# Kernel optimization log

Hardware: AMD Instinct MI355X
Metric: run time of the kernel (lower is better)

Reference implementation:

```python
import jax, jax.numpy as jnp
import numpy as np

N_LIG, M_POC = 16384, 32768
E_LIG, E_POC, K_CROSS = 163840, 327680, 8
H = 64
L = 4

silu = jax.nn.silu


def _lin(k, fan_in, fan_out):
    k1, k2 = jax.random.split(k)
    s = 1.0 / np.sqrt(fan_in)
    W = jax.random.uniform(k1, (fan_in, fan_out), jnp.float32, -s, s)
    b = jax.random.uniform(k2, (fan_out,), jnp.float32, -s, s)
    return W, b


def setup_inputs() -> dict:
    key = jax.random.key(0)
    ks = jax.random.split(key, 32)
    inp = {
        'lig_x': jax.random.normal(ks[0], (N_LIG, 3), jnp.float32),
        'lig_h': jax.random.normal(ks[1], (N_LIG, 17), jnp.float32),
        'poc_x': jax.random.normal(ks[2], (M_POC, 3), jnp.float32),
        'poc_h': jax.random.normal(ks[3], (M_POC, 29), jnp.float32),
        'lig_edge_index': jax.random.randint(ks[4], (2, E_LIG), 0, N_LIG, jnp.int32),
        'lig_edge_attr': jax.random.normal(ks[5], (E_LIG, 6), jnp.float32),
        'poc_edge_index': jax.random.randint(ks[6], (2, E_POC), 0, M_POC, jnp.int32),
        'poc_edge_attr': jax.random.normal(ks[7], (E_POC, 16), jnp.float32),
        'cross_edge_index': jnp.stack([
            jax.random.randint(ks[8], (N_LIG * K_CROSS,), 0, M_POC, jnp.int32),
            jax.random.randint(ks[9], (N_LIG * K_CROSS,), 0, N_LIG, jnp.int32)]),
        'cross_edge_attr': jax.random.normal(ks[10], (N_LIG * K_CROSS, 16), jnp.float32),
        't': jax.random.uniform(ks[11], (1,), jnp.float32),
    }
    # embeddings
    inp['lig_emb_W'], inp['lig_emb_b'] = _lin(ks[12], 18, H)
    inp['poc_emb_W'], inp['poc_emb_b'] = _lin(ks[13], 29, H)
    inp['lig_ee_W'], inp['lig_ee_b'] = _lin(ks[14], 6, H)
    inp['poc_ee_W'], inp['poc_ee_b'] = _lin(ks[15], 16, H)
    inp['cross_ee_W'], inp['cross_ee_b'] = _lin(ks[16], 16, H)
    # per-layer params stacked along leading L axis
    def stack(kk, fan_in, fan_out):
        Ws, bs = zip(*[_lin(k, fan_in, fan_out) for k in jax.random.split(kk, L)])
        return jnp.stack(Ws), jnp.stack(bs)
    inp['phi_e_W1'], inp['phi_e_b1'] = stack(ks[17], 2 * H + 1 + H, H)
    inp['phi_e_W2'], inp['phi_e_b2'] = stack(ks[18], H, H)
    inp['phi_x_W1'], inp['phi_x_b1'] = stack(ks[19], H, H)
    inp['phi_x_W2'], inp['phi_x_b2'] = stack(ks[20], H, 1)
    inp['phi_h_W1'], inp['phi_h_b1'] = stack(ks[21], 2 * H, H)
    inp['phi_h_W2'], inp['phi_h_b2'] = stack(ks[22], H, H)
    inp['out_W1'], inp['out_b1'] = _lin(ks[23], H, H)
    inp['out_W2'], inp['out_b2'] = _lin(ks[24], H, 1)
    return inp


def _forward(lig_x, lig_h, poc_x, poc_h, lig_edge_attr, poc_edge_attr,
             cross_edge_attr, t,
             lig_emb_W, lig_emb_b, poc_emb_W, poc_emb_b,
             lig_ee_W, lig_ee_b, poc_ee_W, poc_ee_b, cross_ee_W, cross_ee_b,
             phi_e_W1, phi_e_b1, phi_e_W2, phi_e_b2,
             phi_x_W1, phi_x_b1, phi_x_W2, phi_x_b2,
             phi_h_W1, phi_h_b1, phi_h_W2, phi_h_b2,
             out_W1, out_b1, out_W2, out_b2,
             lig_edge_index, poc_edge_index, cross_edge_index):
    n_lig = lig_h.shape[0]
    n_tot = n_lig + poc_h.shape[0]
    t_feat = jnp.broadcast_to(t.reshape(1, 1), (n_lig, 1))
    h_lig = jnp.concatenate([lig_h, t_feat], -1) @ lig_emb_W + lig_emb_b
    h_poc = poc_h @ poc_emb_W + poc_emb_b
    h = jnp.concatenate([h_lig, h_poc], 0)          # [N, H]
    x = jnp.concatenate([lig_x, poc_x], 0)          # [N, 3]
    src = jnp.concatenate([lig_edge_index[0], poc_edge_index[0] + n_lig,
                           cross_edge_index[0] + n_lig])
    dst = jnp.concatenate([lig_edge_index[1], poc_edge_index[1] + n_lig,
                           cross_edge_index[1]])
    eattr = jnp.concatenate([
        lig_edge_attr @ lig_ee_W + lig_ee_b,
        poc_edge_attr @ poc_ee_W + poc_ee_b,
        cross_edge_attr @ cross_ee_W + cross_ee_b], 0)  # [E, H]
    # True = pocket => coords not updated
    update_mask = jnp.concatenate([
        jnp.ones((n_lig, 1), h.dtype), jnp.zeros((n_tot - n_lig, 1), h.dtype)], 0)
    for i in range(phi_e_W1.shape[0]):
        diff = x[src] - x[dst]                                    # [E, 3]
        dist = jnp.sum(diff * diff, -1, keepdims=True) / 100.0    # [E, 1]
        e_in = jnp.concatenate([h[src], h[dst], dist, eattr], -1) # [E, 2H+1+H]
        m = silu(silu(e_in @ phi_e_W1[i] + phi_e_b1[i]) @ phi_e_W2[i] + phi_e_b2[i])
        cw = jnp.tanh(silu(m @ phi_x_W1[i] + phi_x_b1[i]) @ phi_x_W2[i] + phi_x_b2[i])
        coord_agg = jax.ops.segment_sum(diff * cw, dst, num_segments=n_tot) * update_mask
        msg_agg = jax.ops.segment_sum(m, dst, num_segments=n_tot)
        h = h + silu(jnp.concatenate([h, msg_agg], -1) @ phi_h_W1[i] + phi_h_b1[i]) @ phi_h_W2[i] + phi_h_b2[i]
        x = x + coord_agg
    disp = x[:n_lig] - lig_x
    scale = silu(h[:n_lig] @ out_W1 + out_b1) @ out_W2 + out_b2
    return scale * disp


def reference(lig_x, lig_h, poc_x, poc_h, lig_edge_attr, poc_edge_attr,
              cross_edge_attr, t,
              lig_emb_W, lig_emb_b, poc_emb_W, poc_emb_b,
              lig_ee_W, lig_ee_b, poc_ee_W, poc_ee_b, cross_ee_W, cross_ee_b,
              phi_e_W1, phi_e_b1, phi_e_W2, phi_e_b2,
              phi_x_W1, phi_x_b1, phi_x_W2, phi_x_b2,
              phi_h_W1, phi_h_b1, phi_h_W2, phi_h_b2,
              out_W1, out_b1, out_W2, out_b2,
              lig_edge_index, poc_edge_index, cross_edge_index):
    return _forward(lig_x, lig_h, poc_x, poc_h, lig_edge_attr, poc_edge_attr,
                    cross_edge_attr, t,
                    lig_emb_W, lig_emb_b, poc_emb_W, poc_emb_b,
                    lig_ee_W, lig_ee_b, poc_ee_W, poc_ee_b, cross_ee_W, cross_ee_b,
                    phi_e_W1, phi_e_b1, phi_e_W2, phi_e_b2,
                    phi_x_W1, phi_x_b1, phi_x_W2, phi_x_b2,
                    phi_h_W1, phi_h_b1, phi_h_W2, phi_h_b2,
                    out_W1, out_b1, out_W2, out_b2,
                    lig_edge_index, poc_edge_index, cross_edge_index)
```

## Files before the change

kernel.cpp:

```cpp
#include <hip/hip_runtime.h>

#define N_LIG 16384
#define M_POC 32768
#define N_TOT (N_LIG + M_POC)
#define E_LIG 163840
#define E_POC 327680
#define E_CROSS (N_LIG * 8)
#define E_TOT (E_LIG + E_POC + E_CROSS)
#define TE 16

typedef __bf16 bf16_t;
typedef bf16_t bf16x8 __attribute__((ext_vector_type(8)));
typedef bf16_t bf16x4 __attribute__((ext_vector_type(4)));
typedef bf16_t bf16x2 __attribute__((ext_vector_type(2)));
typedef float f32x4 __attribute__((ext_vector_type(4)));

#define SM 72
#define WAVE_BYTES (1792 + 2304 + 2304 + 256)

__device__ __forceinline__ float fast_rcp(float x) { return __builtin_amdgcn_rcpf(x); }
__device__ __forceinline__ float silu_f(float v) {
    return v * fast_rcp(1.0f + __expf(-v));
}
__device__ __forceinline__ float tanh_f(float v) {
    float a = fabsf(v);
    float t = __expf(-2.0f * a);
    float r = (1.0f - t) * fast_rcp(1.0f + t);
    return copysignf(r, v);
}

__device__ __forceinline__ void atomic_add_f32(float* p, float v) {
    __hip_atomic_fetch_add(p, v, __ATOMIC_RELAXED, __HIP_MEMORY_SCOPE_AGENT);
}

__device__ __forceinline__ void lds_fence() {
    asm volatile("s_waitcnt lgkmcnt(0)" ::: "memory");
}


__global__ void k_build_edges(const int* __restrict__ lig_ei, const int* __restrict__ poc_ei,
                              const int* __restrict__ cross_ei,
                              int* __restrict__ srcA, int* __restrict__ dstA,
                              int* __restrict__ cnt) {
    int e = blockIdx.x * blockDim.x + threadIdx.x;
    if (e >= E_TOT) return;
    int s, d;
    if (e < E_LIG) {
        s = lig_ei[e];
        d = lig_ei[E_LIG + e];
    } else if (e < E_LIG + E_POC) {
        int i = e - E_LIG;
        s = poc_ei[i] + N_LIG;
        d = poc_ei[E_POC + i] + N_LIG;
    } else {
        int i = e - E_LIG - E_POC;
        s = cross_ei[i] + N_LIG;
        d = cross_ei[E_CROSS + i];
    }
    srcA[e] = s;
    dstA[e] = d;
    atomicAdd(&cnt[d], 1);
}

__global__ __launch_bounds__(1024) void k_scan(const int* __restrict__ cnt,
                                               int* __restrict__ rowptr,
                                               int* __restrict__ cursor) {
    __shared__ int sums[1024];
    int tid = threadIdx.x;
    int local[48];
    int s = 0;
    for (int i = 0; i < 48; ++i) { local[i] = s; s += cnt[tid * 48 + i]; }
    sums[tid] = s;
    __syncthreads();
    for (int off = 1; off < 1024; off <<= 1) {
        int v = (tid >= off) ? sums[tid - off] : 0;
        __syncthreads();
        sums[tid] += v;
        __syncthreads();
    }
    int base = (tid == 0) ? 0 : sums[tid - 1];
    for (int i = 0; i < 48; ++i) {
        int v = base + local[i];
        int idx = tid * 48 + i;
        rowptr[idx] = v;
        cursor[idx] = v;
    }
    if (tid == 1023) rowptr[N_TOT] = sums[1023];
}

__global__ void k_scatter(const int* __restrict__ dstA, int* __restrict__ cursor,
                          int* __restrict__ sortedPos) {
    int e = blockIdx.x * blockDim.x + threadIdx.x;
    if (e < E_TOT) sortedPos[e] = atomicAdd(&cursor[dstA[e]], 1);
}

#define PK_G1   (12 * 5 * 4 * 64)
#define PK_G23  (4 * 4 * 4 * 64)
#define PK_WH   (4 * 24 * 64)
#define PK_BEFF (12 * 64)
#define PK_TOT  (PK_G1 + PK_G23 + PK_WH + PK_BEFF)

__global__ void k_pack_all(const float* __restrict__ phi_e_W1, const float* __restrict__ phi_e_b1,
                           const float* __restrict__ lig_ee_W, const float* __restrict__ lig_ee_b,
                           const float* __restrict__ poc_ee_W, const float* __restrict__ poc_ee_b,
                           const float* __restrict__ cross_ee_W, const float* __restrict__ cross_ee_b,
                           const float* __restrict__ phi_e_W2, const float* __restrict__ phi_x_W1,
                           const float* __restrict__ phi_h_W1, const float* __restrict__ phi_h_W2,
                           bf16_t* __restrict__ Bg1, bf16_t* __restrict__ Bg23,
                           bf16_t* __restrict__ WhP, float* __restrict__ beff) {
    int tid = blockIdx.x * blockDim.x + threadIdx.x;
    if (tid < PK_G1) {
        int lt = tid / 1280;
        int rem = tid - lt * 1280;
        int c = rem >> 8;
        int ft = (rem >> 6) & 3;
        int lane = rem & 63;
        int l = lt / 3, t = lt % 3;
        const float* W1l = phi_e_W1 + l * 193 * 64;
        const float* We; int K;
        if (t == 0) { We = lig_ee_W; K = 6; }
        else if (t == 1) { We = poc_ee_W; K = 16; }
        else { We = cross_ee_W; K = 16; }
        int col = ft * 16 + (lane & 15);
        int k0 = c * 32 + (lane >> 4) * 8;
        #pragma unroll
        for (int j = 0; j < 8; ++j) {
            int row = k0 + j;
            float v = 0.0f;
            if (row < 128) v = W1l[row * 64 + col];
            else if (row < 144) {
                int kk = row - 128;
                if (kk < K) {
                    float a = 0.0f;
                    for (int q = 0; q < 64; ++q) a = fmaf(We[kk * 64 + q], W1l[(129 + q) * 64 + col], a);
                    v = a;
                }
            } else if (row == 144) {
                v = W1l[128 * 64 + col];
            }
            Bg1[(size_t)tid * 8 + j] = (bf16_t)v;
        }
    } else if (tid < PK_G1 + PK_G23) {
        int u = tid - PK_G1;
        int lane = u & 63;
        int ft = (u >> 6) & 3;
        int c = (u >> 8) & 3;
        int l = u >> 10;
        const float* W = (c < 2) ? (phi_e_W2 + l * 4096) : (phi_x_W1 + l * 4096);
        int kb = (c & 1) * 32;
        int col = ft * 16 + (lane & 15);
        int k0 = kb + (lane >> 4) * 8;
        #pragma unroll
        for (int j = 0; j < 8; ++j)
            Bg23[(size_t)u * 8 + j] = (bf16_t)W[(k0 + j) * 64 + col];
    } else if (tid < PK_G1 + PK_G23 + PK_WH) {
        int u = tid - PK_G1 - PK_G23;
        int lane = u & 63;
        int frag = (u >> 6) % 24;
        int l = (u >> 6) / 24;
        const float* W; int kc, ft;
        if (frag < 16) { W = phi_h_W1 + l * 128 * 64; kc = frag >> 2; ft = frag & 3; }
        else           { W = phi_h_W2 + l * 64 * 64;  kc = (frag - 16) >> 2; ft = (frag - 16) & 3; }
        int col = ft * 16 + (lane & 15);
        int k0 = kc * 32 + (lane >> 4) * 8;
        #pragma unroll
        for (int j = 0; j < 8; ++j)
            WhP[(size_t)u * 8 + j] = (bf16_t)W[(k0 + j) * 64 + col];
    } else if (tid < PK_TOT) {
        int u = tid - PK_G1 - PK_G23 - PK_WH;
        int j = u & 63;
        int lt = u >> 6;
        int l = lt / 3, t = lt % 3;
        const float* W1l = phi_e_W1 + l * 193 * 64;
        const float* Be = (t == 0) ? lig_ee_b : ((t == 1) ? poc_ee_b : cross_ee_b);
        float v = phi_e_b1[l * 64 + j];
        for (int q = 0; q < 64; ++q) v = fmaf(Be[q], W1l[(129 + q) * 64 + j], v);
        beff[u] = v;
    }
}

__global__ void k_embed(const float* __restrict__ lig_x, const float* __restrict__ lig_h,
                        const float* __restrict__ poc_x, const float* __restrict__ poc_h,
                        const float* __restrict__ t,
                        const float* __restrict__ ligW, const float* __restrict__ ligB,
                        const float* __restrict__ pocW, const float* __restrict__ pocB,
                        float* __restrict__ h, bf16_t* __restrict__ hB, float* __restrict__ x4) {
    int gid = blockIdx.x * blockDim.x + threadIdx.x;
    int n = gid >> 6;
    int lane = gid & 63;
    if (n >= N_TOT) return;
    float a;
    if (n < N_LIG) {
        a = ligB[lane];
        #pragma unroll
        for (int k = 0; k < 17; ++k) a = fmaf(lig_h[n * 17 + k], ligW[k * 64 + lane], a);
        a = fmaf(t[0], ligW[17 * 64 + lane], a);
        if (lane < 4) x4[n * 4 + lane] = (lane < 3) ? lig_x[n * 3 + lane] : 0.0f;
    } else {
        int p = n - N_LIG;
        a = pocB[lane];
        #pragma unroll
        for (int k = 0; k < 29; ++k) a = fmaf(poc_h[p * 29 + k], pocW[k * 64 + lane], a);
        if (lane < 4) x4[n * 4 + lane] = (lane < 3) ? poc_x[p * 3 + lane] : 0.0f;
    }
    h[n * 64 + lane] = a;
    hB[n * 64 + lane] = (bf16_t)a;
}

__global__ __launch_bounds__(256, 6) void k_edge_mfma(
    const bf16_t* __restrict__ hB, const float* __restrict__ x4,
    const int* __restrict__ srcA, const int* __restrict__ dstA,
    const int* __restrict__ sortedPos,
    const float* __restrict__ lig_attr, const float* __restrict__ poc_attr,
    const float* __restrict__ cross_attr,
    const bf16_t* __restrict__ Bg1L,
    const float* __restrict__ beffL,
    const bf16_t* __restrict__ Bg23L,
    const float* __restrict__ b2, const float* __restrict__ bx1,
    const float* __restrict__ Wx2, const float* __restrict__ bx2,
    bf16_t* __restrict__ mBuf, float* __restrict__ coord_agg) {
    __shared__ __align__(16) char lds[4 * WAVE_BYTES];
    const int lane = threadIdx.x & 63;
    const int wave = threadIdx.x >> 6;
    bf16_t* exL = (bf16_t*)(lds + wave * WAVE_BYTES);
    bf16_t* mT1 = (bf16_t*)(lds + wave * WAVE_BYTES + 1792);
    bf16_t* mT2 = (bf16_t*)(lds + wave * WAVE_BYTES + 1792 + 2304);
    float*  dfL = (float*)(lds + wave * WAVE_BYTES + 1792 + 2304 + 2304);
    const int base = (blockIdx.x * 4 + wave) * TE;

    int tt; const float* attrBase; int astride;
    if (base < E_LIG) { tt = 0; attrBase = lig_attr + (size_t)base * 6; astride = 6; }
    else if (base < E_LIG + E_POC) { tt = 1; attrBase = poc_attr + (size_t)(base - E_LIG) * 16; astride = 16; }
    else { tt = 2; attrBase = cross_attr + (size_t)(base - E_LIG - E_POC) * 16; astride = 16; }

    const int edge = lane & 15;
    const int kgrp = lane >> 4;
    const int mrow0 = kgrp * 4;
    const int e16 = base + edge;
    const int sv = srcA[e16];
    const int dv = dstA[e16];
    const int sp = sortedPos[e16];

    bf16x8 bf0 = *(const bf16x8*)(hB + (size_t)sv * 64 + kgrp * 8);
    bf16x8 bf1 = *(const bf16x8*)(hB + (size_t)sv * 64 + 32 + kgrp * 8);
    bf16x8 bf2 = *(const bf16x8*)(hB + (size_t)dv * 64 + kgrp * 8);
    bf16x8 bf3 = *(const bf16x8*)(hB + (size_t)dv * 64 + 32 + kgrp * 8);

    {
        bf16x8 z = {(bf16_t)0.f, (bf16_t)0.f, (bf16_t)0.f, (bf16_t)0.f,
                    (bf16_t)0.f, (bf16_t)0.f, (bf16_t)0.f, (bf16_t)0.f};
        *(bf16x8*)(exL + (lane >> 2) * 56 + (lane & 3) * 8) = z;
    }
    lds_fence();
    if (lane < 16) {
        float4 xs = *(const float4*)(x4 + (size_t)sv * 4);
        float4 xd = *(const float4*)(x4 + (size_t)dv * 4);
        float d0 = xs.x - xd.x;
        float d1 = xs.y - xd.y;
        float d2 = xs.z - xd.z;
        float dist = (d0 * d0 + d1 * d1 + d2 * d2) * 0.01f;
        exL[lane * 56 + 16] = (bf16_t)dist;
        *(float4*)(dfL + lane * 4) = (float4){d0, d1, d2, dist};
        const float* attr = attrBase + lane * astride;
        if (tt == 0) {
            float2 a0 = *(const float2*)(attr);
            float2 a1 = *(const float2*)(attr + 2);
            float2 a2 = *(const float2*)(attr + 4);
            bf16x8 w0 = {(bf16_t)a0.x, (bf16_t)a0.y, (bf16_t)a1.x, (bf16_t)a1.y,
                         (bf16_t)a2.x, (bf16_t)a2.y, (bf16_t)0.f, (bf16_t)0.f};
            *(bf16x8*)(exL + lane * 56) = w0;
        } else {
            float4 a0 = *(const float4*)(attr);
            float4 a1 = *(const float4*)(attr + 4);
            float4 a2 = *(const float4*)(attr + 8);
            float4 a3 = *(const float4*)(attr + 12);
            bf16x8 w0 = {(bf16_t)a0.x, (bf16_t)a0.y, (bf16_t)a0.z, (bf16_t)a0.w,
                         (bf16_t)a1.x, (bf16_t)a1.y, (bf16_t)a1.z, (bf16_t)a1.w};
            bf16x8 w1 = {(bf16_t)a2.x, (bf16_t)a2.y, (bf16_t)a2.z, (bf16_t)a2.w,
                         (bf16_t)a3.x, (bf16_t)a3.y, (bf16_t)a3.z, (bf16_t)a3.w};
            *(bf16x8*)(exL + lane * 56) = w0;
            *(bf16x8*)(exL + lane * 56 + 8) = w1;
        }
    }
    lds_fence();

    const bf16_t* Bg1 = Bg1L + (size_t)tt * 5 * 4 * 512;
    const float* beff = beffL + tt * 64;
    f32x4 acc1[4];
    #pragma unroll
    for (int ft = 0; ft < 4; ++ft) {
        float4 bv = *(const float4*)(beff + ft * 16 + mrow0);
        acc1[ft] = (f32x4){bv.x, bv.y, bv.z, bv.w};
    }
    bf16x8 bf4 = *(const bf16x8*)(exL + edge * 56 + kgrp * 8);
    bf16x8 bdat[5] = {bf0, bf1, bf2, bf3, bf4};
    #pragma unroll
    for (int c = 0; c < 5; ++c) {
        #pragma unroll
        for (int ft = 0; ft < 4; ++ft) {
            bf16x8 wfr = *(const bf16x8*)(Bg1 + ((size_t)(c * 4 + ft) * 64 + lane) * 8);
            acc1[ft] = __builtin_amdgcn_mfma_f32_16x16x32_bf16(wfr, bdat[c], acc1[ft], 0, 0, 0);
        }
    }
    #pragma unroll
    for (int ft = 0; ft < 4; ++ft) {
        bf16x4 v = {(bf16_t)silu_f(acc1[ft][0]), (bf16_t)silu_f(acc1[ft][1]),
                    (bf16_t)silu_f(acc1[ft][2]), (bf16_t)silu_f(acc1[ft][3])};
        *(bf16x4*)(mT1 + edge * SM + ft * 16 + mrow0) = v;
    }
    lds_fence();

    f32x4 acc2[4];
    #pragma unroll
    for (int ft = 0; ft < 4; ++ft) {
        float4 bv = *(const float4*)(b2 + ft * 16 + mrow0);
        acc2[ft] = (f32x4){bv.x, bv.y, bv.z, bv.w};
    }
    bf16x8 m1f0 = *(const bf16x8*)(mT1 + edge * SM + kgrp * 8);
    bf16x8 m1f1 = *(const bf16x8*)(mT1 + edge * SM + 32 + kgrp * 8);
    #pragma unroll
    for (int c = 0; c < 2; ++c) {
        bf16x8 df = (c == 0) ? m1f0 : m1f1;
        #pragma unroll
        for (int ft = 0; ft < 4; ++ft) {
            bf16x8 wfr = *(const bf16x8*)(Bg23L + ((size_t)(c * 4 + ft) * 64 + lane) * 8);
            acc2[ft] = __builtin_amdgcn_mfma_f32_16x16x32_bf16(wfr, df, acc2[ft], 0, 0, 0);
        }
    }
    #pragma unroll
    for (int ft = 0; ft < 4; ++ft) {
        bf16x4 v = {(bf16_t)silu_f(acc2[ft][0]), (bf16_t)silu_f(acc2[ft][1]),
                    (bf16_t)silu_f(acc2[ft][2]), (bf16_t)silu_f(acc2[ft][3])};
        *(bf16x4*)(mT2 + edge * SM + ft * 16 + mrow0) = v;
        *(bf16x4*)(mBuf + (size_t)sp * 64 + ft * 16 + mrow0) = v;
    }
    lds_fence();

    f32x4 acc3[4];
    #pragma unroll
    for (int ft = 0; ft < 4; ++ft) {
        float4 bv = *(const float4*)(bx1 + ft * 16 + mrow0);
        acc3[ft] = (f32x4){bv.x, bv.y, bv.z, bv.w};
    }
    bf16x8 mf0 = *(const bf16x8*)(mT2 + edge * SM + kgrp * 8);
    bf16x8 mf1 = *(const bf16x8*)(mT2 + edge * SM + 32 + kgrp * 8);
    const bf16_t* Bg3 = Bg23L + (size_t)2 * 4 * 512;
    #pragma unroll
    for (int c = 0; c < 2; ++c) {
        bf16x8 df = (c == 0) ? mf0 : mf1;
        #pragma unroll
        for (int ft = 0; ft < 4; ++ft) {
            bf16x8 wfr = *(const bf16x8*)(Bg3 + ((size_t)(c * 4 + ft) * 64 + lane) * 8);
            acc3[ft] = __builtin_amdgcn_mfma_f32_16x16x32_bf16(wfr, df, acc3[ft], 0, 0, 0);
        }
    }

    float s = 0.0f;
    #pragma unroll
    for (int ft = 0; ft < 4; ++ft) {
        float4 wv = *(const float4*)(Wx2 + ft * 16 + mrow0);
        s = fmaf(silu_f(acc3[ft][0]), wv.x, s);
        s = fmaf(silu_f(acc3[ft][1]), wv.y, s);
        s = fmaf(silu_f(acc3[ft][2]), wv.z, s);
        s = fmaf(silu_f(acc3[ft][3]), wv.w, s);
    }
    s += __shfl_xor(s, 16, 64);
    s += __shfl_xor(s, 32, 64);
    const float cw = tanh_f(s + bx2[0]);
    if (dv < N_LIG && kgrp < 3)
        atomic_add_f32(&coord_agg[dv * 3 + kgrp], dfL[edge * 4 + kgrp] * cw);
}

#define NODE_WAVE_BYTES (2304 + 2304)
__global__ __launch_bounds__(256) void k_node(
    float* __restrict__ h, bf16_t* __restrict__ hB, float* __restrict__ x4,
    const bf16_t* __restrict__ mBuf, const int* __restrict__ rowptr,
    float* __restrict__ coord,
    const bf16_t* __restrict__ WhL,
    const float* __restrict__ bh1, const float* __restrict__ bh2) {
    __shared__ __align__(16) char lds[4 * NODE_WAVE_BYTES];
    const int lane = threadIdx.x & 63;
    const int wave = threadIdx.x >> 6;
    bf16_t* msgT = (bf16_t*)(lds + wave * NODE_WAVE_BYTES);
    bf16_t* mid  = (bf16_t*)(lds + wave * NODE_WAVE_BYTES + 2304);
    const int base = (blockIdx.x * 4 + wave) * TE;

    const int node = lane & 15;
    const int kgrp = lane >> 4;
    const int mrow0 = kgrp * 4;
    const int n16 = base + node;

    const int rp0 = rowptr[n16];
    const int rp1 = rowptr[n16 + 1];
    const int f4 = node * 4;
    for (int r = 0; r < TE; ++r) {
        const int s0 = __shfl(rp0, r, 64);
        const int s1 = __shfl(rp1, r, 64);
        float a0 = 0.f, a1 = 0.f, a2 = 0.f, a3 = 0.f;
        for (int i = s0 + kgrp; i < s1; i += 4) {
            bf16x4 v = *(const bf16x4*)(mBuf + (size_t)i * 64 + f4);
            a0 += (float)v[0]; a1 += (float)v[1]; a2 += (float)v[2]; a3 += (float)v[3];
        }
        a0 += __shfl_xor(a0, 16, 64); a1 += __shfl_xor(a1, 16, 64);
        a2 += __shfl_xor(a2, 16, 64); a3 += __shfl_xor(a3, 16, 64);
        a0 += __shfl_xor(a0, 32, 64); a1 += __shfl_xor(a1, 32, 64);
        a2 += __shfl_xor(a2, 32, 64); a3 += __shfl_xor(a3, 32, 64);
        if (lane < 16) {
            bf16x4 v = {(bf16_t)a0, (bf16_t)a1, (bf16_t)a2, (bf16_t)a3};
            *(bf16x4*)(msgT + r * SM + f4) = v;
        }
    }
    lds_fence();

    f32x4 acc[4];
    #pragma unroll
    for (int ft = 0; ft < 4; ++ft) {
        float4 bv = *(const float4*)(bh1 + ft * 16 + mrow0);
        acc[ft] = (f32x4){bv.x, bv.y, bv.z, bv.w};
    }
    bf16x8 d0 = *(const bf16x8*)(hB + (size_t)n16 * 64 + kgrp * 8);
    bf16x8 d1 = *(const bf16x8*)(hB + (size_t)n16 * 64 + 32 + kgrp * 8);
    bf16x8 d2 = *(const bf16x8*)(msgT + node * SM + kgrp * 8);
    bf16x8 d3 = *(const bf16x8*)(msgT + node * SM + 32 + kgrp * 8);
    bf16x8 bdat[4] = {d0, d1, d2, d3};
    #pragma unroll
    for (int c = 0; c < 4; ++c) {
        #pragma unroll
        for (int ft = 0; ft < 4; ++ft) {
            bf16x8 wfr = *(const bf16x8*)(WhL + ((size_t)(c * 4 + ft) * 64 + lane) * 8);
            acc[ft] = __builtin_amdgcn_mfma_f32_16x16x32_bf16(wfr, bdat[c], acc[ft], 0, 0, 0);
        }
    }
    #pragma unroll
    for (int ft = 0; ft < 4; ++ft) {
        bf16x4 v = {(bf16_t)silu_f(acc[ft][0]), (bf16_t)silu_f(acc[ft][1]),
                    (bf16_t)silu_f(acc[ft][2]), (bf16_t)silu_f(acc[ft][3])};
        *(bf16x4*)(mid + node * SM + ft * 16 + mrow0) = v;
    }
    lds_fence();

    f32x4 acc2[4];
    #pragma unroll
    for (int ft = 0; ft < 4; ++ft) {
        float4 bv = *(const float4*)(bh2 + ft * 16 + mrow0);
        acc2[ft] = (f32x4){bv.x, bv.y, bv.z, bv.w};
    }
    bf16x8 g0 = *(const bf16x8*)(mid + node * SM + kgrp * 8);
    bf16x8 g1 = *(const bf16x8*)(mid + node * SM + 32 + kgrp * 8);
    #pragma unroll
    for (int c = 0; c < 2; ++c) {
        bf16x8 df = (c == 0) ? g0 : g1;
        #pragma unroll
        for (int ft = 0; ft < 4; ++ft) {
            bf16x8 wfr = *(const bf16x8*)(WhL + ((size_t)(16 + c * 4 + ft) * 64 + lane) * 8);
            acc2[ft] = __builtin_amdgcn_mfma_f32_16x16x32_bf16(wfr, df, acc2[ft], 0, 0, 0);
        }
    }

    #pragma unroll
    for (int ft = 0; ft < 4; ++ft) {
        float* hp = h + (size_t)n16 * 64 + ft * 16 + mrow0;
        float4 hv = *(const float4*)hp;
        hv.x += acc2[ft][0]; hv.y += acc2[ft][1]; hv.z += acc2[ft][2]; hv.w += acc2[ft][3];
        *(float4*)hp = hv;
        bf16x4 hb = {(bf16_t)hv.x, (bf16_t)hv.y, (bf16_t)hv.z, (bf16_t)hv.w};
        *(bf16x4*)(hB + (size_t)n16 * 64 + ft * 16 + mrow0) = hb;
    }
    if (kgrp < 3) {
        if (n16 < N_LIG) x4[n16 * 4 + kgrp] += coord[n16 * 3 + kgrp];
        coord[n16 * 3 + kgrp] = 0.0f;
    }
}

__global__ void k_out(const float* __restrict__ h, const float* __restrict__ x4,
                      const float* __restrict__ lig_x,
                      const float* __restrict__ oW1, const float* __restrict__ ob1,
                      const float* __restrict__ oW2, const float* __restrict__ ob2,
                      float* __restrict__ out) {
    int gid = blockIdx.x * blockDim.x + threadIdx.x;
    int n = gid >> 6;
    int lane = gid & 63;
    if (n >= N_LIG) return;
    float hv = h[n * 64 + lane];
    float a = ob1[lane];
    #pragma unroll
    for (int k = 0; k < 64; ++k) a = fmaf(__shfl(hv, k, 64), oW1[k * 64 + lane], a);
    float p = silu_f(a) * oW2[lane];
    #pragma unroll
    for (int off = 32; off > 0; off >>= 1) p += __shfl_xor(p, off, 64);
    float scale = p + ob2[0];
    if (lane < 3) out[n * 3 + lane] = scale * (x4[n * 4 + lane] - lig_x[n * 3 + lane]);
}

extern "C" void kernel_launch(void* const* d_in, const int* in_sizes, int n_in,
                              void* d_out, int out_size, void* d_ws, size_t ws_size,
                              hipStream_t stream) {
    const float* lig_x      = (const float*)d_in[0];
    const float* lig_h      = (const float*)d_in[1];
    const float* poc_x      = (const float*)d_in[2];
    const float* poc_h      = (const float*)d_in[3];
    const int*   lig_ei     = (const int*)d_in[4];
    const float* lig_attr   = (const float*)d_in[5];
    const int*   poc_ei     = (const int*)d_in[6];
    const float* poc_attr   = (const float*)d_in[7];
    const int*   cross_ei   = (const int*)d_in[8];
    const float* cross_attr = (const float*)d_in[9];
    const float* t          = (const float*)d_in[10];
    const float* lig_emb_W  = (const float*)d_in[11];
    const float* lig_emb_b  = (const float*)d_in[12];
    const float* poc_emb_W  = (const float*)d_in[13];
    const float* poc_emb_b  = (const float*)d_in[14];
    const float* lig_ee_W   = (const float*)d_in[15];
    const float* lig_ee_b   = (const float*)d_in[16];
    const float* poc_ee_W   = (const float*)d_in[17];
    const float* poc_ee_b   = (const float*)d_in[18];
    const float* cross_ee_W = (const float*)d_in[19];
    const float* cross_ee_b = (const float*)d_in[20];
    const float* phi_e_W1   = (const float*)d_in[21];
    const float* phi_e_b1   = (const float*)d_in[22];
    const float* phi_e_W2   = (const float*)d_in[23];
    const float* phi_e_b2   = (const float*)d_in[24];
    const float* phi_x_W1   = (const float*)d_in[25];
    const float* phi_x_b1   = (const float*)d_in[26];
    const float* phi_x_W2   = (const float*)d_in[27];
    const float* phi_x_b2   = (const float*)d_in[28];
    const float* phi_h_W1   = (const float*)d_in[29];
    const float* phi_h_b1   = (const float*)d_in[30];
    const float* phi_h_W2   = (const float*)d_in[31];
    const float* phi_h_b2   = (const float*)d_in[32];
    const float* out_W1     = (const float*)d_in[33];
    const float* out_b1     = (const float*)d_in[34];
    const float* out_W2     = (const float*)d_in[35];
    const float* out_b2     = (const float*)d_in[36];

    char* p = (char*)d_ws;
    auto carve = [&](size_t bytes) { char* r = p; p += (bytes + 255) & ~(size_t)255; return r; };
    float*  h      = (float*)carve((size_t)N_TOT * 64 * 4);
    bf16_t* hB     = (bf16_t*)carve((size_t)N_TOT * 64 * 2);
    float*  x4     = (float*)carve((size_t)N_TOT * 4 * 4);
    float*  coord  = (float*)carve((size_t)N_TOT * 3 * 4);
    bf16_t* WhP    = (bf16_t*)carve((size_t)4 * 24 * 512 * 2);
    float*  beff   = (float*)carve((size_t)12 * 64 * 4);
    bf16_t* Bg1    = (bf16_t*)carve((size_t)12 * 5 * 4 * 512 * 2);
    bf16_t* Bg23   = (bf16_t*)carve((size_t)4 * 16 * 512 * 2);
    int*    srcA   = (int*)carve((size_t)E_TOT * 4);
    int*    dstA   = (int*)carve((size_t)E_TOT * 4);
    int*    sortedPos = (int*)carve((size_t)E_TOT * 4);
    int*    cnt    = (int*)carve((size_t)N_TOT * 4);
    int*    cursor = (int*)carve((size_t)N_TOT * 4);
    int*    rowptr = (int*)carve((size_t)(N_TOT + 1) * 4);
    bf16_t* mBuf   = (bf16_t*)carve((size_t)E_TOT * 64 * 2);

    hipMemsetAsync(cnt, 0, (size_t)N_TOT * 4, stream);
    hipMemsetAsync(coord, 0, (size_t)N_TOT * 3 * 4, stream);
    k_build_edges<<<E_TOT / 256, 256, 0, stream>>>(lig_ei, poc_ei, cross_ei, srcA, dstA, cnt);
    k_scan<<<1, 1024, 0, stream>>>(cnt, rowptr, cursor);
    k_scatter<<<E_TOT / 256, 256, 0, stream>>>(dstA, cursor, sortedPos);
    k_pack_all<<<(PK_TOT + 255) / 256, 256, 0, stream>>>(
        phi_e_W1, phi_e_b1, lig_ee_W, lig_ee_b, poc_ee_W, poc_ee_b, cross_ee_W, cross_ee_b,
        phi_e_W2, phi_x_W1, phi_h_W1, phi_h_W2, Bg1, Bg23, WhP, beff);
    k_embed<<<(N_TOT * 64) / 256, 256, 0, stream>>>(
        lig_x, lig_h, poc_x, poc_h, t, lig_emb_W, lig_emb_b, poc_emb_W, poc_emb_b, h, hB, x4);

    for (int l = 0; l < 4; ++l) {
        k_edge_mfma<<<E_TOT / 64, 256, 0, stream>>>(
            hB, x4, srcA, dstA, sortedPos, lig_attr, poc_attr, cross_attr,
            Bg1 + (size_t)l * 3 * 5 * 4 * 512, beff + (size_t)l * 3 * 64,
            Bg23 + (size_t)l * 16 * 512,
            phi_e_b2 + l * 64, phi_x_b1 + l * 64,
            phi_x_W2 + l * 64, phi_x_b2 + l,
            mBuf, coord);
        k_node<<<N_TOT / 64, 256, 0, stream>>>(
            h, hB, x4, mBuf, rowptr, coord,
            WhP + (size_t)l * 24 * 512,
            phi_h_b1 + l * 64, phi_h_b2 + l * 64);
    }

    k_out<<<(N_LIG * 64) / 256, 256, 0, stream>>>(
        h, x4, lig_x, out_W1, out_b1, out_W2, out_b2, (float*)d_out);
}
```

Baseline: 858.4 us.

## Process two 16-edge tiles per wave and keep edge features in registers

Each wave in the edge kernel now handles 32 edges as two interleaved MFMA tiles, so every weight fragment load feeds two MFMAs. Edge attributes and distances are built directly in registers and exchanged by shuffle instead of being staged in LDS, and message stores to the sorted buffer become wider. The grid is halved and the occupancy hint is lowered to 4 to allow for the extra registers, which may reduce latency hiding.

```diff
diff --git a/kernel.cpp b/kernel.cpp
--- a/kernel.cpp
+++ b/kernel.cpp
@@ -12,11 +12,10 @@
 typedef __bf16 bf16_t;
 typedef bf16_t bf16x8 __attribute__((ext_vector_type(8)));
 typedef bf16_t bf16x4 __attribute__((ext_vector_type(4)));
-typedef bf16_t bf16x2 __attribute__((ext_vector_type(2)));
 typedef float f32x4 __attribute__((ext_vector_type(4)));
 
 #define SM 72
-#define WAVE_BYTES (1792 + 2304 + 2304 + 256)
+#define EDGE_WAVE_BYTES (32 * SM * 2)
 
 __device__ __forceinline__ float fast_rcp(float x) { return __builtin_amdgcn_rcpf(x); }
 __device__ __forceinline__ float silu_f(float v) {
@@ -207,7 +206,7 @@
     hB[n * 64 + lane] = (bf16_t)a;
 }
 
-__global__ __launch_bounds__(256, 6) void k_edge_mfma(
+__global__ __launch_bounds__(256, 4) void k_edge_mfma(
     const bf16_t* __restrict__ hB, const float* __restrict__ x4,
     const int* __restrict__ srcA, const int* __restrict__ dstA,
     const int* __restrict__ sortedPos,
@@ -219,14 +218,11 @@
     const float* __restrict__ b2, const float* __restrict__ bx1,
     const float* __restrict__ Wx2, const float* __restrict__ bx2,
     bf16_t* __restrict__ mBuf, float* __restrict__ coord_agg) {
-    __shared__ __align__(16) char lds[4 * WAVE_BYTES];
+    __shared__ __align__(16) char lds[4 * EDGE_WAVE_BYTES];
     const int lane = threadIdx.x & 63;
     const int wave = threadIdx.x >> 6;
-    bf16_t* exL = (bf16_t*)(lds + wave * WAVE_BYTES);
-    bf16_t* mT1 = (bf16_t*)(lds + wave * WAVE_BYTES + 1792);
-    bf16_t* mT2 = (bf16_t*)(lds + wave * WAVE_BYTES + 1792 + 2304);
-    float*  dfL = (float*)(lds + wave * WAVE_BYTES + 1792 + 2304 + 2304);
-    const int base = (blockIdx.x * 4 + wave) * TE;
+    bf16_t* mT = (bf16_t*)(lds + wave * EDGE_WAVE_BYTES);
+    const int base = (blockIdx.x * 4 + wave) * 32;
 
     int tt; const float* attrBase; int astride;
     if (base < E_LIG) { tt = 0; attrBase = lig_attr + (size_t)base * 6; astride = 6; }
@@ -236,139 +232,197 @@
     const int edge = lane & 15;
     const int kgrp = lane >> 4;
     const int mrow0 = kgrp * 4;
-    const int e16 = base + edge;
-    const int sv = srcA[e16];
-    const int dv = dstA[e16];
-    const int sp = sortedPos[e16];
-
-    bf16x8 bf0 = *(const bf16x8*)(hB + (size_t)sv * 64 + kgrp * 8);
-    bf16x8 bf1 = *(const bf16x8*)(hB + (size_t)sv * 64 + 32 + kgrp * 8);
-    bf16x8 bf2 = *(const bf16x8*)(hB + (size_t)dv * 64 + kgrp * 8);
-    bf16x8 bf3 = *(const bf16x8*)(hB + (size_t)dv * 64 + 32 + kgrp * 8);
-
-    {
-        bf16x8 z = {(bf16_t)0.f, (bf16_t)0.f, (bf16_t)0.f, (bf16_t)0.f,
-                    (bf16_t)0.f, (bf16_t)0.f, (bf16_t)0.f, (bf16_t)0.f};
-        *(bf16x8*)(exL + (lane >> 2) * 56 + (lane & 3) * 8) = z;
-    }
-    lds_fence();
-    if (lane < 16) {
-        float4 xs = *(const float4*)(x4 + (size_t)sv * 4);
-        float4 xd = *(const float4*)(x4 + (size_t)dv * 4);
-        float d0 = xs.x - xd.x;
-        float d1 = xs.y - xd.y;
-        float d2 = xs.z - xd.z;
-        float dist = (d0 * d0 + d1 * d1 + d2 * d2) * 0.01f;
-        exL[lane * 56 + 16] = (bf16_t)dist;
-        *(float4*)(dfL + lane * 4) = (float4){d0, d1, d2, dist};
-        const float* attr = attrBase + lane * astride;
+    const int e0 = base + edge;
+    const int e1 = base + 16 + edge;
+    const int sv0 = srcA[e0], sv1 = srcA[e1];
+    const int dv0 = dstA[e0], dv1 = dstA[e1];
+    const int sp0 = sortedPos[e0], sp1 = sortedPos[e1];
+
+    bf16x8 hs0a = *(const bf16x8*)(hB + (size_t)sv0 * 64 + kgrp * 8);
+    bf16x8 hs0b = *(const bf16x8*)(hB + (size_t)sv0 * 64 + 32 + kgrp * 8);
+    bf16x8 hd0a = *(const bf16x8*)(hB + (size_t)dv0 * 64 + kgrp * 8);
+    bf16x8 hd0b = *(const bf16x8*)(hB + (size_t)dv0 * 64 + 32 + kgrp * 8);
+    bf16x8 hs1a = *(const bf16x8*)(hB + (size_t)sv1 * 64 + kgrp * 8);
+    bf16x8 hs1b = *(const bf16x8*)(hB + (size_t)sv1 * 64 + 32 + kgrp * 8);
+    bf16x8 hd1a = *(const bf16x8*)(hB + (size_t)dv1 * 64 + kgrp * 8);
+    bf16x8 hd1b = *(const bf16x8*)(hB + (size_t)dv1 * 64 + 32 + kgrp * 8);
+
+    const bf16_t Z = (bf16_t)0.0f;
+    bf16x8 ex0 = {Z, Z, Z, Z, Z, Z, Z, Z};
+    bf16x8 ex1 = {Z, Z, Z, Z, Z, Z, Z, Z};
+    float d0s0 = 0.f, d1s0 = 0.f, d2s0 = 0.f;
+    float d0s1 = 0.f, d1s1 = 0.f, d2s1 = 0.f;
+    if (kgrp == 0) {
+        const float* a0p = attrBase + (size_t)edge * astride;
+        const float* a1p = attrBase + (size_t)(16 + edge) * astride;
         if (tt == 0) {
-            float2 a0 = *(const float2*)(attr);
-            float2 a1 = *(const float2*)(attr + 2);
-            float2 a2 = *(const float2*)(attr + 4);
-            bf16x8 w0 = {(bf16_t)a0.x, (bf16_t)a0.y, (bf16_t)a1.x, (bf16_t)a1.y,
-                         (bf16_t)a2.x, (bf16_t)a2.y, (bf16_t)0.f, (bf16_t)0.f};
-            *(bf16x8*)(exL + lane * 56) = w0;
+            float4 q0 = *(const float4*)a0p;
+            float2 q1 = *(const float2*)(a0p + 4);
+            ex0 = (bf16x8){(bf16_t)q0.x, (bf16_t)q0.y, (bf16_t)q0.z, (bf16_t)q0.w,
+                           (bf16_t)q1.x, (bf16_t)q1.y, Z, Z};
+            float4 r0 = *(const float4*)a1p;
+            float2 r1 = *(const float2*)(a1p + 4);
+            ex1 = (bf16x8){(bf16_t)r0.x, (bf16_t)r0.y, (bf16_t)r0.z, (bf16_t)r0.w,
+                           (bf16_t)r1.x, (bf16_t)r1.y, Z, Z};
         } else {
-            float4 a0 = *(const float4*)(attr);
-            float4 a1 = *(const float4*)(attr + 4);
-            float4 a2 = *(const float4*)(attr + 8);
-            float4 a3 = *(const float4*)(attr + 12);
-            bf16x8 w0 = {(bf16_t)a0.x, (bf16_t)a0.y, (bf16_t)a0.z, (bf16_t)a0.w,
-                         (bf16_t)a1.x, (bf16_t)a1.y, (bf16_t)a1.z, (bf16_t)a1.w};
-            bf16x8 w1 = {(bf16_t)a2.x, (bf16_t)a2.y, (bf16_t)a2.z, (bf16_t)a2.w,
-                         (bf16_t)a3.x, (bf16_t)a3.y, (bf16_t)a3.z, (bf16_t)a3.w};
-            *(bf16x8*)(exL + lane * 56) = w0;
-            *(bf16x8*)(exL + lane * 56 + 8) = w1;
-        }
-    }
-    lds_fence();
+            float4 q0 = *(const float4*)a0p;
+            float4 q1 = *(const float4*)(a0p + 4);
+            ex0 = (bf16x8){(bf16_t)q0.x, (bf16_t)q0.y, (bf16_t)q0.z, (bf16_t)q0.w,
+                           (bf16_t)q1.x, (bf16_t)q1.y, (bf16_t)q1.z, (bf16_t)q1.w};
+            float4 r0 = *(const float4*)a1p;
+            float4 r1 = *(const float4*)(a1p + 4);
+            ex1 = (bf16x8){(bf16_t)r0.x, (bf16_t)r0.y, (bf16_t)r0.z, (bf16_t)r0.w,
+                           (bf16_t)r1.x, (bf16_t)r1.y, (bf16_t)r1.z, (bf16_t)r1.w};
+        }
+    } else if (kgrp == 1) {
+        if (tt != 0) {
+            const float* a0p = attrBase + (size_t)edge * astride + 8;
+            const float* a1p = attrBase + (size_t)(16 + edge) * astride + 8;
+            float4 q0 = *(const float4*)a0p;
+            float4 q1 = *(const float4*)(a0p + 4);
+            ex0 = (bf16x8){(bf16_t)q0.x, (bf16_t)q0.y, (bf16_t)q0.z, (bf16_t)q0.w,
+                           (bf16_t)q1.x, (bf16_t)q1.y, (bf16_t)q1.z, (bf16_t)q1.w};
+            float4 r0 = *(const float4*)a1p;
+            float4 r1 = *(const float4*)(a1p + 4);
+            ex1 = (bf16x8){(bf16_t)r0.x, (bf16_t)r0.y, (bf16_t)r0.z, (bf16_t)r0.w,
+                           (bf16_t)r1.x, (bf16_t)r1.y, (bf16_t)r1.z, (bf16_t)r1.w};
+        }
+    } else if (kgrp == 2) {
+        float4 xs0 = *(const float4*)(x4 + (size_t)sv0 * 4);
+        float4 xd0 = *(const float4*)(x4 + (size_t)dv0 * 4);
+        float4 xs1 = *(const float4*)(x4 + (size_t)sv1 * 4);
+        float4 xd1 = *(const float4*)(x4 + (size_t)dv1 * 4);
+        d0s0 = xs0.x - xd0.x; d1s0 = xs0.y - xd0.y; d2s0 = xs0.z - xd0.z;
+        d0s1 = xs1.x - xd1.x; d1s1 = xs1.y - xd1.y; d2s1 = xs1.z - xd1.z;
+        float dist0 = (d0s0 * d0s0 + d1s0 * d1s0 + d2s0 * d2s0) * 0.01f;
+        float dist1 = (d0s1 * d0s1 + d1s1 * d1s1 + d2s1 * d2s1) * 0.01f;
+        ex0[0] = (bf16_t)dist0;
+        ex1[0] = (bf16_t)dist1;
+    }
 
     const bf16_t* Bg1 = Bg1L + (size_t)tt * 5 * 4 * 512;
     const float* beff = beffL + tt * 64;
-    f32x4 acc1[4];
+    f32x4 acc0[4], acc1[4];
     #pragma unroll
     for (int ft = 0; ft < 4; ++ft) {
         float4 bv = *(const float4*)(beff + ft * 16 + mrow0);
-        acc1[ft] = (f32x4){bv.x, bv.y, bv.z, bv.w};
-    }
-    bf16x8 bf4 = *(const bf16x8*)(exL + edge * 56 + kgrp * 8);
-    bf16x8 bdat[5] = {bf0, bf1, bf2, bf3, bf4};
+        acc0[ft] = (f32x4){bv.x, bv.y, bv.z, bv.w};
+        acc1[ft] = acc0[ft];
+    }
+    bf16x8 bdat0[5] = {hs0a, hs0b, hd0a, hd0b, ex0};
+    bf16x8 bdat1[5] = {hs1a, hs1b, hd1a, hd1b, ex1};
     #pragma unroll
     for (int c = 0; c < 5; ++c) {
         #pragma unroll
         for (int ft = 0; ft < 4; ++ft) {
             bf16x8 wfr = *(const bf16x8*)(Bg1 + ((size_t)(c * 4 + ft) * 64 + lane) * 8);
-            acc1[ft] = __builtin_amdgcn_mfma_f32_16x16x32_bf16(wfr, bdat[c], acc1[ft], 0, 0, 0);
-        }
-    }
-    #pragma unroll
-    for (int ft = 0; ft < 4; ++ft) {
-        bf16x4 v = {(bf16_t)silu_f(acc1[ft][0]), (bf16_t)silu_f(acc1[ft][1]),
-                    (bf16_t)silu_f(acc1[ft][2]), (bf16_t)silu_f(acc1[ft][3])};
-        *(bf16x4*)(mT1 + edge * SM + ft * 16 + mrow0) = v;
+            acc0[ft] = __builtin_amdgcn_mfma_f32_16x16x32_bf16(wfr, bdat0[c], acc0[ft], 0, 0, 0);
+            acc1[ft] = __builtin_amdgcn_mfma_f32_16x16x32_bf16(wfr, bdat1[c], acc1[ft], 0, 0, 0);
+        }
+    }
+    #pragma unroll
+    for (int ft = 0; ft < 4; ++ft) {
+        bf16x4 v0 = {(bf16_t)silu_f(acc0[ft][0]), (bf16_t)silu_f(acc0[ft][1]),
+                     (bf16_t)silu_f(acc0[ft][2]), (bf16_t)silu_f(acc0[ft][3])};
+        bf16x4 v1 = {(bf16_t)silu_f(acc1[ft][0]), (bf16_t)silu_f(acc1[ft][1]),
+                     (bf16_t)silu_f(acc1[ft][2]), (bf16_t)silu_f(acc1[ft][3])};
+        *(bf16x4*)(mT + edge * SM + ft * 16 + mrow0) = v0;
+        *(bf16x4*)(mT + (16 + edge) * SM + ft * 16 + mrow0) = v1;
     }
     lds_fence();
 
-    f32x4 acc2[4];
+    f32x4 acc20[4], acc21[4];
     #pragma unroll
     for (int ft = 0; ft < 4; ++ft) {
         float4 bv = *(const float4*)(b2 + ft * 16 + mrow0);
-        acc2[ft] = (f32x4){bv.x, bv.y, bv.z, bv.w};
-    }
-    bf16x8 m1f0 = *(const bf16x8*)(mT1 + edge * SM + kgrp * 8);
-    bf16x8 m1f1 = *(const bf16x8*)(mT1 + edge * SM + 32 + kgrp * 8);
+        acc20[ft] = (f32x4){bv.x, bv.y, bv.z, bv.w};
+        acc21[ft] = acc20[ft];
+    }
+    bf16x8 m10[2], m11[2];
     #pragma unroll
     for (int c = 0; c < 2; ++c) {
-        bf16x8 df = (c == 0) ? m1f0 : m1f1;
+        m10[c] = *(const bf16x8*)(mT + edge * SM + c * 32 + kgrp * 8);
+        m11[c] = *(const bf16x8*)(mT + (16 + edge) * SM + c * 32 + kgrp * 8);
+    }
+    #pragma unroll
+    for (int c = 0; c < 2; ++c) {
         #pragma unroll
         for (int ft = 0; ft < 4; ++ft) {
             bf16x8 wfr = *(const bf16x8*)(Bg23L + ((size_t)(c * 4 + ft) * 64 + lane) * 8);
-            acc2[ft] = __builtin_amdgcn_mfma_f32_16x16x32_bf16(wfr, df, acc2[ft], 0, 0, 0);
-        }
-    }
-    #pragma unroll
-    for (int ft = 0; ft < 4; ++ft) {
-        bf16x4 v = {(bf16_t)silu_f(acc2[ft][0]), (bf16_t)silu_f(acc2[ft][1]),
-                    (bf16_t)silu_f(acc2[ft][2]), (bf16_t)silu_f(acc2[ft][3])};
-        *(bf16x4*)(mT2 + edge * SM + ft * 16 + mrow0) = v;
-        *(bf16x4*)(mBuf + (size_t)sp * 64 + ft * 16 + mrow0) = v;
+            acc20[ft] = __builtin_amdgcn_mfma_f32_16x16x32_bf16(wfr, m10[c], acc20[ft], 0, 0, 0);
+            acc21[ft] = __builtin_amdgcn_mfma_f32_16x16x32_bf16(wfr, m11[c], acc21[ft], 0, 0, 0);
+        }
     }
     lds_fence();
-
-    f32x4 acc3[4];
+    #pragma unroll
+    for (int ft = 0; ft < 4; ++ft) {
+        bf16x4 v0 = {(bf16_t)silu_f(acc20[ft][0]), (bf16_t)silu_f(acc20[ft][1]),
+                     (bf16_t)silu_f(acc20[ft][2]), (bf16_t)silu_f(acc20[ft][3])};
+        bf16x4 v1 = {(bf16_t)silu_f(acc21[ft][0]), (bf16_t)silu_f(acc21[ft][1]),
+                     (bf16_t)silu_f(acc21[ft][2]), (bf16_t)silu_f(acc21[ft][3])};
+        *(bf16x4*)(mT + edge * SM + ft * 16 + mrow0) = v0;
+        *(bf16x4*)(mT + (16 + edge) * SM + ft * 16 + mrow0) = v1;
+    }
+    lds_fence();
+
+    bf16x8 g0[2], g1[2];
+    #pragma unroll
+    for (int c = 0; c < 2; ++c) {
+        g0[c] = *(const bf16x8*)(mT + edge * SM + c * 32 + kgrp * 8);
+        g1[c] = *(const bf16x8*)(mT + (16 + edge) * SM + c * 32 + kgrp * 8);
+        *(bf16x8*)(mBuf + (size_t)sp0 * 64 + c * 32 + kgrp * 8) = g0[c];
+        *(bf16x8*)(mBuf + (size_t)sp1 * 64 + c * 32 + kgrp * 8) = g1[c];
+    }
+
+    f32x4 acc30[4], acc31[4];
     #pragma unroll
     for (int ft = 0; ft < 4; ++ft) {
         float4 bv = *(const float4*)(bx1 + ft * 16 + mrow0);
-        acc3[ft] = (f32x4){bv.x, bv.y, bv.z, bv.w};
-    }
-    bf16x8 mf0 = *(const bf16x8*)(mT2 + edge * SM + kgrp * 8);
-    bf16x8 mf1 = *(const bf16x8*)(mT2 + edge * SM + 32 + kgrp * 8);
+        acc30[ft] = (f32x4){bv.x, bv.y, bv.z, bv.w};
+        acc31[ft] = acc30[ft];
+    }
     const bf16_t* Bg3 = Bg23L + (size_t)2 * 4 * 512;
     #pragma unroll
     for (int c = 0; c < 2; ++c) {
-        bf16x8 df = (c == 0) ? mf0 : mf1;
         #pragma unroll
         for (int ft = 0; ft < 4; ++ft) {
             bf16x8 wfr = *(const bf16x8*)(Bg3 + ((size_t)(c * 4 + ft) * 64 + lane) * 8);
-            acc3[ft] = __builtin_amdgcn_mfma_f32_16x16x32_bf16(wfr, df, acc3[ft], 0, 0, 0);
-        }
-    }
-
-    float s = 0.0f;
+            acc30[ft] = __builtin_amdgcn_mfma_f32_16x16x32_bf16(wfr, g0[c], acc30[ft], 0, 0, 0);
+            acc31[ft] = __builtin_amdgcn_mfma_f32_16x16x32_bf16(wfr, g1[c], acc31[ft], 0, 0, 0);
+        }
+    }
+
+    float s0 = 0.0f, s1 = 0.0f;
     #pragma unroll
     for (int ft = 0; ft < 4; ++ft) {
         float4 wv = *(const float4*)(Wx2 + ft * 16 + mrow0);
-        s = fmaf(silu_f(acc3[ft][0]), wv.x, s);
-        s = fmaf(silu_f(acc3[ft][1]), wv.y, s);
-        s = fmaf(silu_f(acc3[ft][2]), wv.z, s);
-        s = fmaf(silu_f(acc3[ft][3]), wv.w, s);
-    }
-    s += __shfl_xor(s, 16, 64);
-    s += __shfl_xor(s, 32, 64);
-    const float cw = tanh_f(s + bx2[0]);
-    if (dv < N_LIG && kgrp < 3)
-        atomic_add_f32(&coord_agg[dv * 3 + kgrp], dfL[edge * 4 + kgrp] * cw);
+        s0 = fmaf(silu_f(acc30[ft][0]), wv.x, s0);
+        s0 = fmaf(silu_f(acc30[ft][1]), wv.y, s0);
+        s0 = fmaf(silu_f(acc30[ft][2]), wv.z, s0);
+        s0 = fmaf(silu_f(acc30[ft][3]), wv.w, s0);
+        s1 = fmaf(silu_f(acc31[ft][0]), wv.x, s1);
+        s1 = fmaf(silu_f(acc31[ft][1]), wv.y, s1);
+        s1 = fmaf(silu_f(acc31[ft][2]), wv.z, s1);
+        s1 = fmaf(silu_f(acc31[ft][3]), wv.w, s1);
+    }
+    s0 += __shfl_xor(s0, 16, 64); s0 += __shfl_xor(s0, 32, 64);
+    s1 += __shfl_xor(s1, 16, 64); s1 += __shfl_xor(s1, 32, 64);
+    const float bx2v = bx2[0];
+    const float cw0 = tanh_f(s0 + bx2v);
+    const float cw1 = tanh_f(s1 + bx2v);
+
+    float a0 = __shfl(d0s0, 32 + edge, 64);
+    float a1 = __shfl(d1s0, 32 + edge, 64);
+    float a2 = __shfl(d2s0, 32 + edge, 64);
+    float b0 = __shfl(d0s1, 32 + edge, 64);
+    float b1 = __shfl(d1s1, 32 + edge, 64);
+    float b2v_ = __shfl(d2s1, 32 + edge, 64);
+    if (kgrp < 3) {
+        float dsel0 = (kgrp == 0) ? a0 : ((kgrp == 1) ? a1 : a2);
+        float dsel1 = (kgrp == 0) ? b0 : ((kgrp == 1) ? b1 : b2v_);
+        if (dv0 < N_LIG) atomic_add_f32(&coord_agg[dv0 * 3 + kgrp], dsel0 * cw0);
+        if (dv1 < N_LIG) atomic_add_f32(&coord_agg[dv1 * 3 + kgrp], dsel1 * cw1);
+    }
 }
 
 #define NODE_WAVE_BYTES (2304 + 2304)
@@ -563,7 +617,7 @@
         lig_x, lig_h, poc_x, poc_h, t, lig_emb_W, lig_emb_b, poc_emb_W, poc_emb_b, h, hB, x4);
 
     for (int l = 0; l < 4; ++l) {
-        k_edge_mfma<<<E_TOT / 64, 256, 0, stream>>>(
+        k_edge_mfma<<<E_TOT / 128, 256, 0, stream>>>(
             hB, x4, srcA, dstA, sortedPos, lig_attr, poc_attr, cross_attr,
             Bg1 + (size_t)l * 3 * 5 * 4 * 512, beff + (size_t)l * 3 * 64,
             Bg23 + (size_t)l * 16 * 512,
```

After: 748.1 us. -12.8%, faster.
